# Performance work log

Hardware: AMD Instinct MI355X
Metric: run time of the kernel (lower is better)

The kernel has to match this reference:

```python
import jax, jax.numpy as jnp
import numpy as np

TEMPERATURE = 8.0  # sqrt(d_k) with d_k = 64
EPS = 1e-8


def setup_inputs() -> dict:
    key = jax.random.key(0)
    kq, kk, kv, km = jax.random.split(key, 4)
    B, L, D = 16, 2048, 64
    q = jax.random.normal(kq, (B, L, D), dtype=jnp.float32)
    k = jax.random.normal(kk, (B, L, D), dtype=jnp.float32)
    v = jax.random.normal(kv, (B, L, D), dtype=jnp.float32)
    # True entries are zeroed out AFTER softmax (post-softmax masking)
    mask = jax.random.randint(km, (B, L, L), 0, 2).astype(jnp.bool_)
    return {"q": q, "k": k, "v": v, "mask": mask}


def reference(q, k, v, mask):
    # attn scores: [B, Lq, Lk]
    attn = jnp.einsum("bqd,bkd->bqk", q, k) / TEMPERATURE
    attn = jax.nn.softmax(attn, axis=2)
    # post-softmax masking followed by renormalization (breaks flash-attn fusion)
    attn = jnp.where(mask, 0.0, attn)
    attn = attn / (jnp.sum(attn, axis=2, keepdims=True) + EPS)
    # dropout is identity in eval/reference mode
    output = jnp.einsum("bqk,bkd->bqd", attn, v)
    return output, attn
```

## Files before the change

kernel.cpp:

```cpp
#include <hip/hip_runtime.h>

#define BATCH 16
#define LSEQ 2048
#define DIM 64
#define TQ 32
#define SSTRIDE 2056
#define EPSV 1e-8f
#define SCALE_LOG2E 0.18033688011112042f

typedef float f4 __attribute__((ext_vector_type(4)));
typedef _Float16 h4 __attribute__((ext_vector_type(4)));
typedef _Float16 h8 __attribute__((ext_vector_type(8)));
typedef int i4t __attribute__((ext_vector_type(4)));

__device__ inline h8 cvt_h8(f4 a, f4 b) {
    h8 r;
    r[0] = (_Float16)a[0]; r[1] = (_Float16)a[1];
    r[2] = (_Float16)a[2]; r[3] = (_Float16)a[3];
    r[4] = (_Float16)b[0]; r[5] = (_Float16)b[1];
    r[6] = (_Float16)b[2]; r[7] = (_Float16)b[3];
    return r;
}

__global__ __launch_bounds__(256)
void cvt_k_kernel(const float* __restrict__ k, _Float16* __restrict__ kh) {
    const int idx = blockIdx.x * 256 + threadIdx.x;
    f4 v = ((const f4*)k)[idx];
    h4 h;
    #pragma unroll
    for (int e = 0; e < 4; ++e) h[e] = (_Float16)v[e];
    ((h4*)kh)[idx] = h;
}

__global__ __launch_bounds__(256)
void tr_v_kernel(const float* __restrict__ v, _Float16* __restrict__ vt) {
    __shared__ float tile[64][65];
    const int b = blockIdx.y, k0 = blockIdx.x * 64, t = threadIdx.x;
    const float* vb = v + ((size_t)b * LSEQ + k0) * DIM;
    #pragma unroll
    for (int p = 0; p < 4; ++p) {
        const int row = p * 16 + (t >> 4), c4 = (t & 15) * 4;
        f4 val = *(const f4*)(vb + row * DIM + c4);
        #pragma unroll
        for (int e = 0; e < 4; ++e) tile[row][c4 + e] = val[e];
    }
    __syncthreads();
    _Float16* vtb = vt + (size_t)b * DIM * LSEQ;
    #pragma unroll
    for (int p = 0; p < 4; ++p) {
        const int d = p * 16 + (t >> 4), k4 = (t & 15) * 4;
        h4 h;
        #pragma unroll
        for (int e = 0; e < 4; ++e) h[e] = (_Float16)tile[k4 + e][d];
        *(h4*)(vtb + (size_t)d * LSEQ + k0 + k4) = h;
    }
}

__global__ __launch_bounds__(1024, 4)
void attn_kernel(const float* __restrict__ q, const _Float16* __restrict__ kh,
                 const _Float16* __restrict__ vt, const int* __restrict__ mask,
                 float* __restrict__ out, float* __restrict__ attn)
{
    __shared__ __align__(16) _Float16 s_p[TQ][SSTRIDE];
    __shared__ float oacc[16][256];
    __shared__ float s_inv[TQ];

    const int b    = blockIdx.y;
    const int q0   = blockIdx.x * TQ;
    const int tid  = threadIdx.x;
    const int w    = tid >> 6;
    const int lane = tid & 63;
    const int quad = lane >> 4;
    const int m16  = lane & 15;

    const int row0 = 2 * w;
    const int* mrow0 = mask + ((size_t)b * LSEQ + q0 + row0) * LSEQ;
    i4t mv0[8];
    #pragma unroll
    for (int j = 0; j < 8; ++j)
        mv0[j] = __builtin_nontemporal_load((const i4t*)(mrow0 + lane * 4 + 256 * j));

    const float* qrowA = q + ((size_t)b * LSEQ + q0 + m16) * DIM + quad * 8;
    const float* qrowB = qrowA + 16 * DIM;
    h8 aqA0 = cvt_h8(*(const f4*)(qrowA),      *(const f4*)(qrowA + 4));
    h8 aqA1 = cvt_h8(*(const f4*)(qrowA + 32), *(const f4*)(qrowA + 36));
    h8 aqB0 = cvt_h8(*(const f4*)(qrowB),      *(const f4*)(qrowB + 4));
    h8 aqB1 = cvt_h8(*(const f4*)(qrowB + 32), *(const f4*)(qrowB + 36));

    for (int t = w; t < LSEQ / 16; t += 16) {
        const int c = t * 16;
        const _Float16* krow = kh + ((size_t)b * LSEQ + c + m16) * DIM + quad * 8;
        h8 bk0 = *(const h8*)(krow);
        h8 bk1 = *(const h8*)(krow + 32);
        f4 accA = {0.f, 0.f, 0.f, 0.f}, accB = {0.f, 0.f, 0.f, 0.f};
        accA = __builtin_amdgcn_mfma_f32_16x16x32_f16(aqA0, bk0, accA, 0, 0, 0);
        accA = __builtin_amdgcn_mfma_f32_16x16x32_f16(aqA1, bk1, accA, 0, 0, 0);
        accB = __builtin_amdgcn_mfma_f32_16x16x32_f16(aqB0, bk0, accB, 0, 0, 0);
        accB = __builtin_amdgcn_mfma_f32_16x16x32_f16(aqB1, bk1, accB, 0, 0, 0);
        #pragma unroll
        for (int r = 0; r < 4; ++r) {
            s_p[quad * 4 + r][c + m16]      = (_Float16)(accA[r] * SCALE_LOG2E);
            s_p[16 + quad * 4 + r][c + m16] = (_Float16)(accB[r] * SCALE_LOG2E);
        }
    }
    __syncthreads();

    const int* mrow1 = mrow0 + LSEQ;
    i4t mv1[8];
    #pragma unroll
    for (int j = 0; j < 8; ++j)
        mv1[j] = __builtin_nontemporal_load((const i4t*)(mrow1 + lane * 4 + 256 * j));

    #pragma unroll
    for (int rr = 0; rr < 2; ++rr) {
        const int row = 2 * w + rr;
        float sa = 0.f, sk = 0.f;
        h4 pk[8];
        #pragma unroll
        for (int j = 0; j < 8; ++j) {
            h4 hv = *(const h4*)(&s_p[row][lane * 4 + 256 * j]);
            i4t m = rr ? mv1[j] : mv0[j];
            #pragma unroll
            for (int e = 0; e < 4; ++e) {
                float p = exp2f((float)hv[e]);
                sa += p;
                float pm = m[e] ? 0.f : p;
                sk += pm;
                pk[j][e] = (_Float16)pm;
            }
        }
        #pragma unroll
        for (int off = 32; off >= 1; off >>= 1) {
            sa += __shfl_xor(sa, off);
            sk += __shfl_xor(sk, off);
        }
        const float inv_d = 1.f / (sk + EPSV * sa);
        if (lane == 0) s_inv[row] = inv_d;

        float* arow = attn + ((size_t)b * LSEQ + q0 + row) * LSEQ;
        #pragma unroll
        for (int j = 0; j < 8; ++j) {
            const int c = lane * 4 + 256 * j;
            *(h4*)(&s_p[row][c]) = pk[j];
            f4 pv;
            #pragma unroll
            for (int e = 0; e < 4; ++e) pv[e] = inv_d * (float)pk[j][e];
            __builtin_nontemporal_store(pv, (f4*)(&arow[c]));
        }
    }
    __syncthreads();

    const int dt = w & 3;
    const int kq = w >> 2;
    const _Float16* vtr = vt + ((size_t)b * DIM + dt * 16 + m16) * LSEQ;
    f4 accA = {0.f, 0.f, 0.f, 0.f}, accB = {0.f, 0.f, 0.f, 0.f};
    #pragma unroll 2
    for (int kb = kq * 512; kb < kq * 512 + 512; kb += 32) {
        const int kk = kb + quad * 8;
        h8 bf  = *(const h8*)(vtr + kk);
        h8 afA = *(const h8*)(&s_p[m16][kk]);
        h8 afB = *(const h8*)(&s_p[16 + m16][kk]);
        accA = __builtin_amdgcn_mfma_f32_16x16x32_f16(afA, bf, accA, 0, 0, 0);
        accB = __builtin_amdgcn_mfma_f32_16x16x32_f16(afB, bf, accB, 0, 0, 0);
    }

    float* ob = out + ((size_t)b * LSEQ + q0) * DIM;

    #pragma unroll
    for (int r = 0; r < 4; ++r)
        oacc[w][(quad * 4 + r) * 16 + m16] = accA[r];
    __syncthreads();
    {
        const int row = tid >> 6;
        const int d   = tid & 63;
        const int dt2 = d >> 4, dc = d & 15;
        const int o   = row * 16 + dc;
        float vsum = oacc[dt2][o] + oacc[4 + dt2][o]
                   + oacc[8 + dt2][o] + oacc[12 + dt2][o];
        ob[row * DIM + d] = s_inv[row] * vsum;
    }
    __syncthreads();

    #pragma unroll
    for (int r = 0; r < 4; ++r)
        oacc[w][(quad * 4 + r) * 16 + m16] = accB[r];
    __syncthreads();
    {
        const int row = tid >> 6;
        const int d   = tid & 63;
        const int dt2 = d >> 4, dc = d & 15;
        const int o   = row * 16 + dc;
        float vsum = oacc[dt2][o] + oacc[4 + dt2][o]
                   + oacc[8 + dt2][o] + oacc[12 + dt2][o];
        ob[(16 + row) * DIM + d] = s_inv[16 + row] * vsum;
    }
}

__global__ __launch_bounds__(512, 4)
void attn_kernel_fb(const float* __restrict__ q, const float* __restrict__ k,
                    const float* __restrict__ v, const int* __restrict__ mask,
                    float* __restrict__ out, float* __restrict__ attn)
{
    __shared__ __align__(16) _Float16 s_p[16][SSTRIDE];
    __shared__ float oacc[8][16 * 16];
    __shared__ float s_inv[16];

    const int b = blockIdx.y, q0 = blockIdx.x * 16, tid = threadIdx.x;
    const int w = tid >> 6, lane = tid & 63, quad = lane >> 4, m16 = lane & 15;
    const float* kp = k + (size_t)b * LSEQ * DIM;
    const float* vp = v + (size_t)b * LSEQ * DIM;
    const float* qrow = q + ((size_t)b * LSEQ + q0 + m16) * DIM + quad * 8;
    h8 aq0 = cvt_h8(*(const f4*)(qrow),      *(const f4*)(qrow + 4));
    h8 aq1 = cvt_h8(*(const f4*)(qrow + 32), *(const f4*)(qrow + 36));

    for (int t = w; t < LSEQ / 16; t += 8) {
        const int c = t * 16;
        const float* krow = kp + (size_t)(c + m16) * DIM + quad * 8;
        h8 bk0 = cvt_h8(*(const f4*)(krow),      *(const f4*)(krow + 4));
        h8 bk1 = cvt_h8(*(const f4*)(krow + 32), *(const f4*)(krow + 36));
        f4 acc = {0.f, 0.f, 0.f, 0.f};
        acc = __builtin_amdgcn_mfma_f32_16x16x32_f16(aq0, bk0, acc, 0, 0, 0);
        acc = __builtin_amdgcn_mfma_f32_16x16x32_f16(aq1, bk1, acc, 0, 0, 0);
        #pragma unroll
        for (int r = 0; r < 4; ++r)
            s_p[quad * 4 + r][c + m16] = (_Float16)(acc[r] * 0.125f);
    }
    __syncthreads();

    #pragma unroll
    for (int rr = 0; rr < 2; ++rr) {
        const int row = 2 * w + rr;
        const int* mrow = mask + ((size_t)b * LSEQ + q0 + row) * LSEQ;
        i4t mv[8];
        #pragma unroll
        for (int j = 0; j < 8; ++j)
            mv[j] = __builtin_nontemporal_load((const i4t*)(mrow + lane * 4 + 256 * j));
        float sa = 0.f, sk = 0.f;
        h4 pk[8];
        #pragma unroll
        for (int j = 0; j < 8; ++j) {
            h4 hv = *(const h4*)(&s_p[row][lane * 4 + 256 * j]);
            #pragma unroll
            for (int e = 0; e < 4; ++e) {
                float p = __expf((float)hv[e]);
                sa += p;
                float pm = mv[j][e] ? 0.f : p;
                sk += pm;
                pk[j][e] = (_Float16)pm;
            }
        }
        #pragma unroll
        for (int off = 32; off >= 1; off >>= 1) {
            sa += __shfl_xor(sa, off);
            sk += __shfl_xor(sk, off);
        }
        const float inv_d = 1.f / (sk + EPSV * sa);
        if (lane == 0) s_inv[row] = inv_d;
        float* arow = attn + ((size_t)b * LSEQ + q0 + row) * LSEQ;
        #pragma unroll
        for (int j = 0; j < 8; ++j) {
            const int c = lane * 4 + 256 * j;
            *(h4*)(&s_p[row][c]) = pk[j];
            f4 pv;
            #pragma unroll
            for (int e = 0; e < 4; ++e) pv[e] = inv_d * (float)pk[j][e];
            __builtin_nontemporal_store(pv, (f4*)(&arow[c]));
        }
    }
    __syncthreads();

    {
        const int dt = w >> 1, kh_ = w & 1;
        f4 acc = {0.f, 0.f, 0.f, 0.f};
        for (int kb0 = kh_ * 1024; kb0 < kh_ * 1024 + 1024; kb0 += 32) {
            const int kk = kb0 + quad * 8;
            h8 af = *(const h8*)(&s_p[m16][kk]);
            const float* vcol = vp + (size_t)kk * DIM + dt * 16 + m16;
            h8 bf;
            #pragma unroll
            for (int j = 0; j < 8; ++j) bf[j] = (_Float16)vcol[j * DIM];
            acc = __builtin_amdgcn_mfma_f32_16x16x32_f16(af, bf, acc, 0, 0, 0);
        }
        #pragma unroll
        for (int r = 0; r < 4; ++r)
            oacc[w][(quad * 4 + r) * 16 + m16] = acc[r];
    }
    __syncthreads();

    float* ob = out + ((size_t)b * LSEQ + q0) * DIM;
    #pragma unroll
    for (int it = 0; it < 2; ++it) {
        const int idx = tid + it * 512;
        const int row = idx >> 6, d = idx & 63;
        const int dt2 = d >> 4, dc = d & 15;
        ob[row * DIM + d] = s_inv[row] *
            (oacc[2 * dt2][row * 16 + dc] + oacc[2 * dt2 + 1][row * 16 + dc]);
    }
}

extern "C" void kernel_launch(void* const* d_in, const int* in_sizes, int n_in,
                              void* d_out, int out_size, void* d_ws, size_t ws_size,
                              hipStream_t stream) {
    const float* q = (const float*)d_in[0];
    const float* k = (const float*)d_in[1];
    const float* v = (const float*)d_in[2];
    const int* mask = (const int*)d_in[3];
    float* out = (float*)d_out;
    float* attn = out + (size_t)BATCH * LSEQ * DIM;

    const size_t kv_elems = (size_t)BATCH * LSEQ * DIM;
    if (ws_size >= kv_elems * 2 * sizeof(_Float16)) {
        _Float16* kh = (_Float16*)d_ws;
        _Float16* vt = kh + kv_elems;
        cvt_k_kernel<<<kv_elems / 4 / 256, 256, 0, stream>>>(k, kh);
        tr_v_kernel<<<dim3(LSEQ / 64, BATCH), 256, 0, stream>>>(v, vt);
        attn_kernel<<<dim3(LSEQ / TQ, BATCH), 1024, 0, stream>>>(q, kh, vt, mask, out, attn);
    } else {
        attn_kernel_fb<<<dim3(LSEQ / 16, BATCH), 512, 0, stream>>>(q, k, v, mask, out, attn);
    }
}
```

Baseline: 499.7 us.

## Defer attn stores past PV MFMA, use LDS-only barriers and fast exp2

```diff
diff --git a/kernel.cpp b/kernel.cpp
--- a/kernel.cpp
+++ b/kernel.cpp
@@ -20,6 +20,20 @@
     r[4] = (_Float16)b[0]; r[5] = (_Float16)b[1];
     r[6] = (_Float16)b[2]; r[7] = (_Float16)b[3];
     return r;
+}
+
+__device__ inline float fast_exp2(float x) {
+#if __has_builtin(__builtin_amdgcn_exp2f)
+    return __builtin_amdgcn_exp2f(x);
+#else
+    return exp2f(x);
+#endif
+}
+
+__device__ inline void lds_barrier() {
+    asm volatile("s_waitcnt lgkmcnt(0)" ::: "memory");
+    __builtin_amdgcn_s_barrier();
+    __builtin_amdgcn_sched_barrier(0);
 }
 
 __global__ __launch_bounds__(256)
@@ -73,8 +87,7 @@
     const int quad = lane >> 4;
     const int m16  = lane & 15;
 
-    const int row0 = 2 * w;
-    const int* mrow0 = mask + ((size_t)b * LSEQ + q0 + row0) * LSEQ;
+    const int* mrow0 = mask + ((size_t)b * LSEQ + q0 + 2 * w) * LSEQ;
     i4t mv0[8];
     #pragma unroll
     for (int j = 0; j < 8; ++j)
@@ -87,8 +100,9 @@
     h8 aqB0 = cvt_h8(*(const f4*)(qrowB),      *(const f4*)(qrowB + 4));
     h8 aqB1 = cvt_h8(*(const f4*)(qrowB + 32), *(const f4*)(qrowB + 36));
 
-    for (int t = w; t < LSEQ / 16; t += 16) {
-        const int c = t * 16;
+    #pragma unroll 2
+    for (int i = 0; i < 8; ++i) {
+        const int c = w * 16 + i * 256;
         const _Float16* krow = kh + ((size_t)b * LSEQ + c + m16) * DIM + quad * 8;
         h8 bk0 = *(const h8*)(krow);
         h8 bk1 = *(const h8*)(krow + 32);
@@ -103,7 +117,6 @@
             s_p[16 + quad * 4 + r][c + m16] = (_Float16)(accB[r] * SCALE_LOG2E);
         }
     }
-    __syncthreads();
 
     const int* mrow1 = mrow0 + LSEQ;
     i4t mv1[8];
@@ -111,6 +124,9 @@
     for (int j = 0; j < 8; ++j)
         mv1[j] = __builtin_nontemporal_load((const i4t*)(mrow1 + lane * 4 + 256 * j));
 
+    lds_barrier();
+
+    float inv0 = 0.f, inv1 = 0.f;
     #pragma unroll
     for (int rr = 0; rr < 2; ++rr) {
         const int row = 2 * w + rr;
@@ -122,7 +138,7 @@
             i4t m = rr ? mv1[j] : mv0[j];
             #pragma unroll
             for (int e = 0; e < 4; ++e) {
-                float p = exp2f((float)hv[e]);
+                float p = fast_exp2((float)hv[e]);
                 sa += p;
                 float pm = m[e] ? 0.f : p;
                 sk += pm;
@@ -135,26 +151,20 @@
             sk += __shfl_xor(sk, off);
         }
         const float inv_d = 1.f / (sk + EPSV * sa);
+        if (rr == 0) inv0 = inv_d; else inv1 = inv_d;
         if (lane == 0) s_inv[row] = inv_d;
-
-        float* arow = attn + ((size_t)b * LSEQ + q0 + row) * LSEQ;
-        #pragma unroll
-        for (int j = 0; j < 8; ++j) {
-            const int c = lane * 4 + 256 * j;
-            *(h4*)(&s_p[row][c]) = pk[j];
-            f4 pv;
-            #pragma unroll
-            for (int e = 0; e < 4; ++e) pv[e] = inv_d * (float)pk[j][e];
-            __builtin_nontemporal_store(pv, (f4*)(&arow[c]));
-        }
-    }
-    __syncthreads();
+        #pragma unroll
+        for (int j = 0; j < 8; ++j)
+            *(h4*)(&s_p[row][lane * 4 + 256 * j]) = pk[j];
+    }
+
+    lds_barrier();
 
     const int dt = w & 3;
     const int kq = w >> 2;
     const _Float16* vtr = vt + ((size_t)b * DIM + dt * 16 + m16) * LSEQ;
     f4 accA = {0.f, 0.f, 0.f, 0.f}, accB = {0.f, 0.f, 0.f, 0.f};
-    #pragma unroll 2
+    #pragma unroll 4
     for (int kb = kq * 512; kb < kq * 512 + 512; kb += 32) {
         const int kk = kb + quad * 8;
         h8 bf  = *(const h8*)(vtr + kk);
@@ -164,12 +174,28 @@
         accB = __builtin_amdgcn_mfma_f32_16x16x32_f16(afB, bf, accB, 0, 0, 0);
     }
 
+    #pragma unroll
+    for (int rr = 0; rr < 2; ++rr) {
+        const int row = 2 * w + rr;
+        const float ivd = rr ? inv1 : inv0;
+        float* arow = attn + ((size_t)b * LSEQ + q0 + row) * LSEQ;
+        #pragma unroll
+        for (int j = 0; j < 8; ++j) {
+            const int c = lane * 4 + 256 * j;
+            h4 hv = *(const h4*)(&s_p[row][c]);
+            f4 pv;
+            #pragma unroll
+            for (int e = 0; e < 4; ++e) pv[e] = ivd * (float)hv[e];
+            __builtin_nontemporal_store(pv, (f4*)(&arow[c]));
+        }
+    }
+
     float* ob = out + ((size_t)b * LSEQ + q0) * DIM;
 
     #pragma unroll
     for (int r = 0; r < 4; ++r)
         oacc[w][(quad * 4 + r) * 16 + m16] = accA[r];
-    __syncthreads();
+    lds_barrier();
     {
         const int row = tid >> 6;
         const int d   = tid & 63;
@@ -179,12 +205,12 @@
                    + oacc[8 + dt2][o] + oacc[12 + dt2][o];
         ob[row * DIM + d] = s_inv[row] * vsum;
     }
-    __syncthreads();
+    lds_barrier();
 
     #pragma unroll
     for (int r = 0; r < 4; ++r)
         oacc[w][(quad * 4 + r) * 16 + m16] = accB[r];
-    __syncthreads();
+    lds_barrier();
     {
         const int row = tid >> 6;
         const int d   = tid & 63;
```

After: 499.7 us. About the same (+0.0%).
